# Kernel tuning notes

Measured on AMD Instinct MI355X. Metric: run time of the kernel, lower is better.

## Reference

```python
import jax, jax.numpy as jnp
import numpy as np

B, D_IN, D_HID, D_OUT = 16384, 512, 512, 512
E, K = 8, 2
VQ_COEFF, LB_COEFF = 0.05, 0.01
LOG100 = float(np.log(100.0))
LOG2 = float(np.log(2.0))


def _normalize(v):
    # torch F.normalize(dim=1): x / max(||x||, 1e-12)
    n = jnp.linalg.norm(v, axis=-1, keepdims=True)
    return v / jnp.maximum(n, 1e-12)


def _cv_squared(v):
    # torch .var() is unbiased (ddof=1)
    return jnp.var(v, ddof=1) / (jnp.mean(v) ** 2 + 1e-10)


def _rbm_layer(x, rm, W, b, ca, temp):
    # x: [B, d_in], rm: [E, d_in], W: [E, d_out, d_in], b: [E, d_out]
    rm_n = jax.lax.stop_gradient(_normalize(rm))          # .detach() in source
    nx = _normalize(x)
    dists = nx @ rm_n.T                                    # [B, E]
    top_v, top_i = jax.lax.top_k(dists, K)                 # [B, K]
    tv = jax.nn.softmax(top_v, axis=-1)                    # softmax over top-k
    bsz = dists.shape[0]
    attn = jnp.zeros_like(dists).at[jnp.arange(bsz)[:, None], top_i].set(tv)
    # const_attention is frozen (requires_grad=False)
    inp_att = jnp.exp(jnp.minimum(jax.lax.stop_gradient(ca), LOG100))  # [E]
    # dense gather-compute-scatter: expert e output for every token, masked by attn
    eo = jnp.einsum('bi,eoi->beo', x, W) * inp_att[None, :, None] + b[None, :, :]
    out = jnp.einsum('be,beo->bo', jax.lax.stop_gradient(attn), eo)    # att.detach()
    out = out * jnp.exp(jnp.minimum(temp, LOG100))
    # aux losses (eval mode: no EMA memory update)
    vq = -(nx[:, None, :] * rm_n[top_i]).sum(-1)           # [B, K]
    vq_loss = (tv * vq).sum(-1).mean()
    lb = _cv_squared(attn.sum(0))
    aux = VQ_COEFF * vq_loss + LB_COEFF * lb               # sim_coeff = 0
    return out, aux


def setup_inputs() -> dict:
    key = jax.random.key(0)
    ks = jax.random.split(key, 8)
    x = jax.random.normal(ks[0], (B, D_IN), dtype=jnp.float32)
    rm0 = _normalize(jax.random.normal(ks[1], (E, D_IN), dtype=jnp.float32))
    W0 = jax.random.normal(ks[2], (E, D_HID, D_IN), dtype=jnp.float32) / np.sqrt(D_IN)
    b0 = jnp.zeros((E, D_HID), dtype=jnp.float32)
    rm1 = _normalize(jax.random.normal(ks[3], (E, D_HID), dtype=jnp.float32))
    W1 = jax.random.normal(ks[4], (E, D_OUT, D_HID), dtype=jnp.float32) / np.sqrt(D_HID)
    b1 = jnp.zeros((E, D_OUT), dtype=jnp.float32)
    temp0 = jnp.full((1,), LOG2, dtype=jnp.float32)
    temp1 = jnp.full((1,), LOG2, dtype=jnp.float32)
    ca0 = jnp.zeros((E,), dtype=jnp.float32)
    ca1 = jnp.zeros((E,), dtype=jnp.float32)
    return {"x": x, "rm0": rm0, "W0": W0, "b0": b0, "temp0": temp0, "ca0": ca0,
            "rm1": rm1, "W1": W1, "b1": b1, "temp1": temp1, "ca1": ca1}


def reference(x, rm0, W0, b0, temp0, ca0, rm1, W1, b1, temp1, ca1):
    h0, a0 = _rbm_layer(x, rm0, W0, b0, ca0, temp0)
    h_emb = h0                      # embedding tapped after layer 0 (pre-activation)
    h = jax.nn.relu(h0)             # norm_type=None -> no norm
    h1, a1 = _rbm_layer(h, rm1, W1, b1, ca1, temp1)
    return (h_emb, h1, a0 + a1)
```

## Files before the change

kernel.cpp:

```cpp
#include <hip/hip_runtime.h>
#include <cmath>
#include <cstdint>

#define NTOK   16384
#define NEXP   8
#define DM     512
#define LOG100 4.605170185988092f

typedef _Float16 half8  __attribute__((ext_vector_type(8)));
typedef float    floatx4 __attribute__((ext_vector_type(4)));

#define MFMA_F16(a, b, c) __builtin_amdgcn_mfma_f32_16x16x32_f16((a), (b), (c), 0, 0, 0)

__device__ __forceinline__ void gl_lds16(const void* g, void* l) {
    __builtin_amdgcn_global_load_lds(
        (const __attribute__((address_space(1))) void*)g,
        (__attribute__((address_space(3))) void*)l, 16, 0, 0);
}


__global__ __launch_bounds__(256) void prep_kernel(
    const float* __restrict__ rm0, const float* __restrict__ rm1,
    const float* __restrict__ ca0, const float* __restrict__ ca1,
    const float* __restrict__ temp0, const float* __restrict__ temp1,
    float* __restrict__ ctrl, float* __restrict__ rmn)
{
    int tid = threadIdx.x, lane = tid & 63, w = tid >> 6;
    if (tid < 32) ((int*)ctrl)[tid] = 0;
    if (tid >= 32 && tid < 48) ctrl[tid] = 0.f;
    if (tid == 48 || tid == 49) ctrl[tid] = 0.f;
    if (tid == 50) ctrl[50] = expf(fminf(temp0[0], LOG100));
    if (tid == 51) ctrl[51] = expf(fminf(temp1[0], LOG100));
    if (tid >= 52 && tid < 68) {
        int i = tid - 52;
        ctrl[tid] = expf(fminf(i < 8 ? ca0[i] : ca1[i - 8], LOG100));
    }
    for (int r = w; r < 16; r += 4) {
        const float* src = (r < 8) ? (rm0 + r * DM) : (rm1 + (r - 8) * DM);
        float v[8]; float ss = 0.f;
        #pragma unroll
        for (int j = 0; j < 8; ++j) { v[j] = src[lane + 64 * j]; ss += v[j] * v[j]; }
        #pragma unroll
        for (int off = 32; off > 0; off >>= 1) ss += __shfl_xor(ss, off);
        float inv = 1.f / fmaxf(sqrtf(ss), 1e-12f);
        float* dst = rmn + r * DM;
        #pragma unroll
        for (int j = 0; j < 8; ++j) dst[lane + 64 * j] = v[j] * inv;
    }
}

__global__ __launch_bounds__(256) void pack_w_kernel(
    const float* __restrict__ W0, const float* __restrict__ W1,
    half8* __restrict__ w0pk, half8* __restrict__ w1pk)
{
    int i = blockIdx.x * 256 + threadIdx.x;
    if (i < 512 * 1024) {
        int l = i & 63, j = (i >> 6) & 15, kb = (i >> 10) & 15, nt = (i >> 14) & 3, e = i >> 16;
        int s = l >> 3, p = l & 7, c = p ^ s;
        int n = nt * 128 + j * 8 + s;
        int k = kb * 32 + (c & 3) * 8;
        const float* src = W0 + ((size_t)e * DM + n) * DM + k;
        half8 v;
        #pragma unroll
        for (int t = 0; t < 8; ++t) {
            float f = src[t];
            _Float16 h = (_Float16)f;
            v[t] = (c < 4) ? h : (_Float16)(f - (float)h);
        }
        w0pk[i] = v;
    } else {
        int m = i - 512 * 1024;
        int l = m & 63, j = (m >> 6) & 15, kb = (m >> 10) & 7, nt = (m >> 13) & 3, e = m >> 15;
        int s = l >> 3, p = l & 7, c = p ^ s;
        int n = nt * 128 + j * 8 + s;
        int k = kb * 64 + c * 8;
        const float* src = W1 + ((size_t)e * DM + n) * DM + k;
        half8 v;
        #pragma unroll
        for (int t = 0; t < 8; ++t) v[t] = (_Float16)src[t];
        w1pk[m] = v;
    }
}

__global__ __launch_bounds__(256) void route_kernel(
    const float* __restrict__ src,
    const float* __restrict__ rmn,
    int relu_in, int split,
    _Float16* __restrict__ dst,
    unsigned char* __restrict__ key,
    float2* __restrict__ wts,
    float2* __restrict__ bs)
{
    __shared__ float rmLds[NEXP * DM];
    int tid = threadIdx.x;
    for (int i = tid; i < NEXP * DM; i += 256) rmLds[i] = rmn[i];
    __syncthreads();
    int lane = tid & 63, w = tid >> 6;
    int token = blockIdx.x * 4 + w;

    const float* row = src + (size_t)token * DM;
    float x[8]; float ss = 0.f;
    #pragma unroll
    for (int j = 0; j < 8; ++j) {
        float v = row[lane + 64 * j];
        if (relu_in) v = fmaxf(v, 0.f);
        x[j] = v; ss += v * v;
    }
    if (split) {
        #pragma unroll
        for (int j = 0; j < 8; ++j) {
            int k = lane + 64 * j;
            size_t base = (size_t)token * 1024 + (size_t)((k >> 5) << 6) + (k & 31);
            _Float16 h = (_Float16)x[j];
            dst[base] = h;
            dst[base + 32] = (_Float16)(x[j] - (float)h);
        }
    } else {
        #pragma unroll
        for (int j = 0; j < 8; ++j)
            dst[(size_t)token * DM + lane + 64 * j] = (_Float16)x[j];
    }
    float d[8];
    #pragma unroll
    for (int e = 0; e < 8; ++e) {
        float a = 0.f;
        #pragma unroll
        for (int j = 0; j < 8; ++j) a += x[j] * rmLds[e * DM + lane + 64 * j];
        d[e] = a;
    }
    #pragma unroll
    for (int off = 32; off > 0; off >>= 1) {
        ss += __shfl_xor(ss, off);
        #pragma unroll
        for (int e = 0; e < 8; ++e) d[e] += __shfl_xor(d[e], off);
    }
    float inv = 1.f / fmaxf(sqrtf(ss), 1e-12f);
    float best = -1e30f, second = -1e30f; int be = 0, se = 0;
    #pragma unroll
    for (int e = 0; e < 8; ++e) {
        float de = d[e] * inv;
        if (de > best)        { second = best; se = be; best = de; be = e; }
        else if (de > second) { second = de; se = e; }
    }
    float z = expf(second - best);
    float w0 = 1.f / (1.f + z), w1 = z / (1.f + z);
    if (lane == 0) {
        key[token] = (unsigned char)be;
        key[NTOK + token] = (unsigned char)se;
        wts[token] = make_float2(w0, w1);
        bs[token] = make_float2(best, second);
    }
}

__global__ __launch_bounds__(256) void compact_kernel(
    const unsigned char* __restrict__ key,
    const float2* __restrict__ wts,
    const float2* __restrict__ bs,
    int* __restrict__ cnt,
    unsigned short* __restrict__ bkt,
    float* __restrict__ imp,
    float* __restrict__ vq_acc)
{
    int slot = blockIdx.x >> 3, e = blockIdx.x & 7;
    int chunk = blockIdx.y;
    const unsigned char* k = key + slot * NTOK;
    unsigned short* ob = bkt + (size_t)(slot * 8 + e) * NTOK;
    int tid = threadIdx.x, lane = tid & 63, w = tid >> 6;
    float wsum = 0.f, vqs = 0.f;
    for (int c = 0; c < 8; ++c) {
        int tok = chunk * 2048 + c * 256 + tid;
        bool m = (k[tok] == (unsigned char)e);
        unsigned long long mask = __ballot(m);
        int wcount = __popcll(mask);
        int wbase = 0;
        if (lane == 0 && wcount) wbase = atomicAdd(&cnt[slot * 8 + e], wcount);
        wbase = __shfl(wbase, 0);
        if (m) {
            int pre = __popcll(mask & ((1ull << lane) - 1ull));
            ob[wbase + pre] = (unsigned short)tok;
            float2 wp = wts[tok]; float2 b2 = bs[tok];
            float wv = slot ? wp.y : wp.x;
            wsum += wv;
            vqs  += wv * (slot ? b2.y : b2.x);
        }
    }
    #pragma unroll
    for (int off = 32; off > 0; off >>= 1) {
        wsum += __shfl_xor(wsum, off);
        vqs  += __shfl_xor(vqs, off);
    }
    __shared__ float rw[4], rv[4];
    if (lane == 0) { rw[w] = wsum; rv[w] = vqs; }
    __syncthreads();
    if (tid == 0) {
        atomicAdd(&imp[e], rw[0] + rw[1] + rw[2] + rw[3]);
        atomicAdd(vq_acc, -(rv[0] + rv[1] + rv[2] + rv[3]));
    }
}

template <bool SPLIT>
__global__ __launch_bounds__(256) void gemm_kernel(
    const _Float16* __restrict__ A,
    const _Float16* __restrict__ Wpk,
    const float* __restrict__ bias,
    const float* __restrict__ iav,
    const float* __restrict__ tscp,
    const int* __restrict__ cnt,
    const unsigned short* __restrict__ bkt,
    const float2* __restrict__ wts,
    int slot, int accum,
    float* __restrict__ outp)
{
    __shared__ __align__(16) _Float16 lds[2 * 16384];
    __shared__ int tokLds[128];

    int t = blockIdx.x;
    int e = -1, m0 = 0, M = 0, acc = 0;
    #pragma unroll
    for (int ee = 0; ee < 8; ++ee) {
        int Me = cnt[ee];
        int ne = (Me + 127) >> 7;
        if (t >= acc && t < acc + ne) { e = ee; m0 = (t - acc) << 7; M = Me; }
        acc += ne;
    }
    if (e < 0) return;
    int nt = blockIdx.y, n0 = nt << 7;
    int valid = min(128, M - m0);
    int tid = threadIdx.x, lane = tid & 63, w = tid >> 6;
    if (tid < 128) tokLds[tid] = bkt[e * NTOK + m0 + min(tid, valid - 1)];
    __syncthreads();

    int subRow = lane >> 3, p = lane & 7;
    int cSt = p ^ subRow;
    int wm = w >> 1, wn = w & 1;
    int r0 = wm * 64, c0 = wn * 64;
    int q = lane >> 4, l15 = lane & 15;

    constexpr int KIT = SPLIT ? 16 : 8;
    constexpr int AS  = SPLIT ? 1024 : 512;

    int tokR[4];
    #pragma unroll
    for (int jj = 0; jj < 4; ++jj) tokR[jj] = tokLds[(w + jj * 4) * 8 + subRow];

    const _Float16* wtile = Wpk + (size_t)(e * 4 + nt) * KIT * 8192;

    floatx4 accu[4][4];
    #pragma unroll
    for (int mi = 0; mi < 4; ++mi)
        #pragma unroll
        for (int ni = 0; ni < 4; ++ni) accu[mi][ni] = (floatx4){0.f, 0.f, 0.f, 0.f};

    auto stage = [&](int kb, int buf) {
        _Float16* dA = lds + buf * 16384;
        _Float16* dB = dA + 8192;
        #pragma unroll
        for (int jj = 0; jj < 4; ++jj) {
            int j = w + jj * 4;
            gl_lds16(A + (size_t)tokR[jj] * AS + kb * 64 + cSt * 8, (void*)(dA + j * 512));
        }
        const _Float16* wb = wtile + (size_t)kb * 8192;
        #pragma unroll
        for (int jj = 0; jj < 4; ++jj) {
            int j = w + jj * 4;
            gl_lds16(wb + j * 512 + lane * 8, (void*)(dB + j * 512));
        }
    };

    auto compute = [&](int buf) {
        const _Float16* bA = lds + buf * 16384;
        const _Float16* bB = bA + 8192;
        if constexpr (SPLIT) {
            half8 ah[4], al[4];
            #pragma unroll
            for (int mi = 0; mi < 4; ++mi) {
                int r = r0 + mi * 16 + l15;
                int ph = q ^ (r & 7), pl = (q + 4) ^ (r & 7);
                ah[mi] = *(const half8*)(bA + r * 64 + ph * 8);
                al[mi] = *(const half8*)(bA + r * 64 + pl * 8);
            }
            #pragma unroll
            for (int ni = 0; ni < 4; ++ni) {
                int r = c0 + ni * 16 + l15;
                int ph = q ^ (r & 7), pl = (q + 4) ^ (r & 7);
                half8 bh = *(const half8*)(bB + r * 64 + ph * 8);
                half8 bl = *(const half8*)(bB + r * 64 + pl * 8);
                #pragma unroll
                for (int mi = 0; mi < 4; ++mi) accu[mi][ni] = MFMA_F16(ah[mi], bh, accu[mi][ni]);
                #pragma unroll
                for (int mi = 0; mi < 4; ++mi) accu[mi][ni] = MFMA_F16(ah[mi], bl, accu[mi][ni]);
                #pragma unroll
                for (int mi = 0; mi < 4; ++mi) accu[mi][ni] = MFMA_F16(al[mi], bh, accu[mi][ni]);
            }
        } else {
            #pragma unroll
            for (int ks = 0; ks < 2; ++ks) {
                half8 a[4];
                #pragma unroll
                for (int mi = 0; mi < 4; ++mi) {
                    int r = r0 + mi * 16 + l15;
                    int pc = (ks * 4 + q) ^ (r & 7);
                    a[mi] = *(const half8*)(bA + r * 64 + pc * 8);
                }
                #pragma unroll
                for (int ni = 0; ni < 4; ++ni) {
                    int r = c0 + ni * 16 + l15;
                    int pc = (ks * 4 + q) ^ (r & 7);
                    half8 b = *(const half8*)(bB + r * 64 + pc * 8);
                    #pragma unroll
                    for (int mi = 0; mi < 4; ++mi) accu[mi][ni] = MFMA_F16(a[mi], b, accu[mi][ni]);
                }
            }
        }
    };

    stage(0, 0);
    __syncthreads();
    int cur = 0;
    for (int kb = 0; kb < KIT - 1; ++kb) {
        stage(kb + 1, cur ^ 1);
        compute(cur);
        __syncthreads();
        cur ^= 1;
    }
    compute(cur);

    float tsc = *tscp, iae = iav[e];
    float bv[4];
    #pragma unroll
    for (int ni = 0; ni < 4; ++ni) bv[ni] = bias[e * DM + n0 + c0 + ni * 16 + l15];
    #pragma unroll
    for (int mi = 0; mi < 4; ++mi) {
        int liBase = r0 + mi * 16 + q * 4;
        #pragma unroll
        for (int reg = 0; reg < 4; ++reg) {
            int li = liBase + reg;
            if (li < valid) {
                int tok = tokLds[li];
                float2 wp = wts[tok];
                float wgt = slot ? wp.y : wp.x;
                float sg = tsc * wgt * iae, sb = tsc * wgt;
                float* orow = outp + (size_t)tok * DM + n0;
                #pragma unroll
                for (int ni = 0; ni < 4; ++ni) {
                    float v = accu[mi][ni][reg] * sg + bv[ni] * sb;
                    int c = c0 + ni * 16 + l15;
                    if (accum) orow[c] += v; else orow[c] = v;
                }
            }
        }
    }
}

__global__ void finalize_kernel(const float* __restrict__ ctrl, float* __restrict__ outp)
{
    if (threadIdx.x == 0) {
        float aux = 0.f;
        for (int l = 0; l < 2; ++l) {
            float vq = ctrl[48 + l] / (float)NTOK;
            float mean = 0.f;
            for (int e = 0; e < 8; ++e) mean += ctrl[32 + l * 8 + e];
            mean *= 0.125f;
            float s = 0.f;
            for (int e = 0; e < 8; ++e) {
                float d = ctrl[32 + l * 8 + e] - mean;
                s += d * d;
            }
            float var = s / 7.f;
            float lb = var / (mean * mean + 1e-10f);
            aux += 0.05f * vq + 0.01f * lb;
        }
        *outp = aux;
    }
}

extern "C" void kernel_launch(void* const* d_in, const int* in_sizes, int n_in,
                              void* d_out, int out_size, void* d_ws, size_t ws_size,
                              hipStream_t stream) {
    const float* x     = (const float*)d_in[0];
    const float* rm0   = (const float*)d_in[1];
    const float* W0    = (const float*)d_in[2];
    const float* b0    = (const float*)d_in[3];
    const float* temp0 = (const float*)d_in[4];
    const float* ca0   = (const float*)d_in[5];
    const float* rm1   = (const float*)d_in[6];
    const float* W1    = (const float*)d_in[7];
    const float* b1    = (const float*)d_in[8];
    const float* temp1 = (const float*)d_in[9];
    const float* ca1   = (const float*)d_in[10];
    float* out = (float*)d_out;

    char* ws = (char*)d_ws;
    float* ctrl = (float*)ws;
    int*   cnt  = (int*)ctrl;
    float* imp  = ctrl + 32;
    float* vq   = ctrl + 48;
    float* tsc  = ctrl + 50;
    float* ia   = ctrl + 52;
    float* rmn  = ctrl + 128;
    float2*        wts = (float2*)(ws + (size_t)64  * 1024);
    float2*        bs  = (float2*)(ws + (size_t)384 * 1024);
    unsigned char* key = (unsigned char*)(ws + (size_t)704 * 1024);

    char* big = ws + (1 << 20);
    half8*          w0pk8 = (half8*)(big);
    half8*          w1pk8 = (half8*)(big + (size_t)8  * 1024 * 1024);
    const _Float16* w0pk  = (const _Float16*)w0pk8;
    const _Float16* w1pk  = (const _Float16*)w1pk8;
    _Float16*       h16   = (_Float16*)(big + (size_t)12 * 1024 * 1024);
    unsigned short* bkt   = (unsigned short*)(big + (size_t)28 * 1024 * 1024);

    _Float16* xpk = (_Float16*)(out + (size_t)NTOK * DM);

    prep_kernel<<<1, 256, 0, stream>>>(rm0, rm1, ca0, ca1, temp0, temp1, ctrl, rmn);
    pack_w_kernel<<<3072, 256, 0, stream>>>(W0, W1, w0pk8, w1pk8);

    route_kernel<<<4096, 256, 0, stream>>>(x, rmn, 0, 1, xpk, key, wts, bs);
    compact_kernel<<<dim3(16, 8), 256, 0, stream>>>(key, wts, bs, cnt, bkt, imp, vq);
    gemm_kernel<true><<<dim3(135, 4), 256, 0, stream>>>(xpk, w0pk, b0, ia, tsc,
        cnt, bkt, wts, 0, 0, out);
    gemm_kernel<true><<<dim3(135, 4), 256, 0, stream>>>(xpk, w0pk, b0, ia, tsc,
        cnt + 8, bkt + 8 * NTOK, wts, 1, 1, out);

    route_kernel<<<4096, 256, 0, stream>>>(out, rmn + 4096, 1, 0, h16,
        key + 2 * NTOK, wts + NTOK, bs + NTOK);
    compact_kernel<<<dim3(16, 8), 256, 0, stream>>>(key + 2 * NTOK, wts + NTOK, bs + NTOK,
        cnt + 16, bkt + 16 * NTOK, imp + 8, vq + 1);
    gemm_kernel<false><<<dim3(135, 4), 256, 0, stream>>>(h16, w1pk, b1, ia + 8, tsc + 1,
        cnt + 16, bkt + 16 * NTOK, wts + NTOK, 0, 0, out + (size_t)NTOK * DM);
    gemm_kernel<false><<<dim3(135, 4), 256, 0, stream>>>(h16, w1pk, b1, ia + 8, tsc + 1,
        cnt + 24, bkt + 24 * NTOK, wts + NTOK, 1, 1, out + (size_t)NTOK * DM);

    finalize_kernel<<<1, 64, 0, stream>>>(ctrl, out + (size_t)2 * NTOK * DM);
}
```

Measured before the change: 486.5 us.

## Remap GEMM blocks by XCD and deepen LDS prefetch pipeline with explicit waitcnt

The grouped GEMM grid becomes 1D with 544 blocks, remapped so consecutive tile rows share an XCD and all four N-tiles of a token tile land on the same XCD. This is meant to improve L2 reuse of the gathered activations. The K loop now issues two stages ahead and replaces __syncthreads with partial vmcnt waits and raw barriers, so global-to-LDS loads overlap compute. The vmcnt(8) count depends on how many loads each stage issues, and it is a correctness risk if that count is wrong.

After: 464.9 us. 1.05x faster.

```diff
diff --git a/kernel.cpp b/kernel.cpp
--- a/kernel.cpp
+++ b/kernel.cpp
@@ -214,7 +214,9 @@
     __shared__ __align__(16) _Float16 lds[2 * 16384];
     __shared__ int tokLds[128];
 
-    int t = blockIdx.x;
+    int p = blockIdx.x;
+    int xcd = p & 7, s = p >> 3;
+    int t = xcd * 17 + (s >> 2), nt = s & 3;
     int e = -1, m0 = 0, M = 0, acc = 0;
     #pragma unroll
     for (int ee = 0; ee < 8; ++ee) {
@@ -224,14 +226,14 @@
         acc += ne;
     }
     if (e < 0) return;
-    int nt = blockIdx.y, n0 = nt << 7;
+    int n0 = nt << 7;
     int valid = min(128, M - m0);
     int tid = threadIdx.x, lane = tid & 63, w = tid >> 6;
     if (tid < 128) tokLds[tid] = bkt[e * NTOK + m0 + min(tid, valid - 1)];
     __syncthreads();
 
-    int subRow = lane >> 3, p = lane & 7;
-    int cSt = p ^ subRow;
+    int subRow = lane >> 3, pp = lane & 7;
+    int cSt = pp ^ subRow;
     int wm = w >> 1, wn = w & 1;
     int r0 = wm * 64, c0 = wn * 64;
     int q = lane >> 4, l15 = lane & 15;
@@ -315,15 +317,20 @@
     };
 
     stage(0, 0);
-    __syncthreads();
-    int cur = 0;
+    stage(1, 1);
     for (int kb = 0; kb < KIT - 1; ++kb) {
-        stage(kb + 1, cur ^ 1);
-        compute(cur);
-        __syncthreads();
-        cur ^= 1;
-    }
-    compute(cur);
+        asm volatile("s_waitcnt vmcnt(8)" ::: "memory");
+        __builtin_amdgcn_s_barrier();
+        __builtin_amdgcn_sched_barrier(0);
+        compute(kb & 1);
+        __builtin_amdgcn_sched_barrier(0);
+        __builtin_amdgcn_s_barrier();
+        if (kb + 2 < KIT) stage(kb + 2, kb & 1);
+    }
+    asm volatile("s_waitcnt vmcnt(0)" ::: "memory");
+    __builtin_amdgcn_s_barrier();
+    __builtin_amdgcn_sched_barrier(0);
+    compute((KIT - 1) & 1);
 
     float tsc = *tscp, iae = iav[e];
     float bv[4];
@@ -417,18 +424,18 @@
 
     route_kernel<<<4096, 256, 0, stream>>>(x, rmn, 0, 1, xpk, key, wts, bs);
     compact_kernel<<<dim3(16, 8), 256, 0, stream>>>(key, wts, bs, cnt, bkt, imp, vq);
-    gemm_kernel<true><<<dim3(135, 4), 256, 0, stream>>>(xpk, w0pk, b0, ia, tsc,
+    gemm_kernel<true><<<544, 256, 0, stream>>>(xpk, w0pk, b0, ia, tsc,
         cnt, bkt, wts, 0, 0, out);
-    gemm_kernel<true><<<dim3(135, 4), 256, 0, stream>>>(xpk, w0pk, b0, ia, tsc,
+    gemm_kernel<true><<<544, 256, 0, stream>>>(xpk, w0pk, b0, ia, tsc,
         cnt + 8, bkt + 8 * NTOK, wts, 1, 1, out);
 
     route_kernel<<<4096, 256, 0, stream>>>(out, rmn + 4096, 1, 0, h16,
         key + 2 * NTOK, wts + NTOK, bs + NTOK);
     compact_kernel<<<dim3(16, 8), 256, 0, stream>>>(key + 2 * NTOK, wts + NTOK, bs + NTOK,
         cnt + 16, bkt + 16 * NTOK, imp + 8, vq + 1);
-    gemm_kernel<false><<<dim3(135, 4), 256, 0, stream>>>(h16, w1pk, b1, ia + 8, tsc + 1,
+    gemm_kernel<false><<<544, 256, 0, stream>>>(h16, w1pk, b1, ia + 8, tsc + 1,
         cnt + 16, bkt + 16 * NTOK, wts + NTOK, 0, 0, out + (size_t)NTOK * DM);
-    gemm_kernel<false><<<dim3(135, 4), 256, 0, stream>>>(h16, w1pk, b1, ia + 8, tsc + 1,
+    gemm_kernel<false><<<544, 256, 0, stream>>>(h16, w1pk, b1, ia + 8, tsc + 1,
         cnt + 24, bkt + 24 * NTOK, wts + NTOK, 1, 1, out + (size_t)NTOK * DM);
 
     finalize_kernel<<<1, 64, 0, stream>>>(ctrl, out + (size_t)2 * NTOK * DM);
```
